# Optimization experiments

Hardware: AMD Instinct MI355X
Metric: run time of the kernel (lower is better)

Reference implementation:

```python
import jax, jax.numpy as jnp
import numpy as np

D = 64      # voxel grid resolution
N = 65536   # active voxels
C = 512     # channels
H = 2048    # mlp hidden = 4*C
EPS = 1e-6


def setup_inputs() -> dict:
    key = jax.random.key(0)
    ks = jax.random.split(key, 8)
    # unique sparse voxel coords (submanifold conv assumes no duplicates)
    rng = np.random.default_rng(0)
    lin = rng.choice(D * D * D, size=N, replace=False)
    coords = jnp.asarray(np.stack([lin // (D * D), (lin // D) % D, lin % D], axis=1), dtype=jnp.int32)  # [N,3]
    s = 1.0 / np.sqrt(C)
    return {
        'feats': jax.random.normal(ks[0], (N, C), jnp.float32),
        'coords': coords,
        'conv_w': jax.random.normal(ks[1], (3, 3, 3, C, C), jnp.float32) * (s / np.sqrt(27.0)),
        'conv_b': jax.random.normal(ks[2], (C,), jnp.float32) * 0.02,
        'ln_g': jnp.ones((C,), jnp.float32),
        'ln_b': jnp.zeros((C,), jnp.float32),
        'w1': jax.random.normal(ks[3], (C, H), jnp.float32) * s,
        'b1': jnp.zeros((H,), jnp.float32),
        'w2': jax.random.normal(ks[4], (H, C), jnp.float32) * (1.0 / np.sqrt(H)),
        'b2': jnp.zeros((C,), jnp.float32),
    }


def _sparse_conv3x3x3(feats, coords, conv_w, conv_b):
    # submanifold sparse conv: out[i] = b + sum_{offsets} feats[nbr(i,off)] @ W[off]
    n = feats.shape[0]
    # padded dense index grid: grid[x+1,y+1,z+1] = voxel row index, -1 = empty
    grid = jnp.full((D + 2, D + 2, D + 2), -1, dtype=jnp.int32)
    grid = grid.at[coords[:, 0] + 1, coords[:, 1] + 1, coords[:, 2] + 1].set(
        jnp.arange(n, dtype=jnp.int32))
    h = jnp.broadcast_to(conv_b, feats.shape).astype(feats.dtype)
    for dx in (0, 1, 2):
        for dy in (0, 1, 2):
            for dz in (0, 1, 2):
                nbr = grid[coords[:, 0] + dx, coords[:, 1] + dy, coords[:, 2] + dz]  # [N]
                valid = (nbr >= 0)
                g = feats[jnp.where(valid, nbr, 0)] * valid[:, None].astype(feats.dtype)  # [N,C]
                h = h + g @ conv_w[dx, dy, dz]
    return h


def reference(feats, coords, conv_w, conv_b, ln_g, ln_b, w1, b1, w2, b2):
    h = _sparse_conv3x3x3(feats, coords, conv_w, conv_b)          # [N,C]
    # LayerNorm32: normalize in fp32, eps=1e-6, affine
    h32 = h.astype(jnp.float32)
    mu = jnp.mean(h32, axis=-1, keepdims=True)
    var = jnp.mean(jnp.square(h32 - mu), axis=-1, keepdims=True)
    nf = ((h32 - mu) * jax.lax.rsqrt(var + EPS) * ln_g + ln_b).astype(feats.dtype)
    # SiLU MLP + residual
    out = jax.nn.silu(nf @ w1 + b1) @ w2 + b2 + feats
    return out
```

## Files before the change

### kernel.cpp

```cpp
#include <hip/hip_runtime.h>

typedef __attribute__((ext_vector_type(8))) short short8;
typedef __attribute__((ext_vector_type(4))) float f32x4;
typedef __attribute__((ext_vector_type(4))) float f4v;
typedef unsigned short u16;
typedef unsigned int u32;

#define NPTS 65536
#define CCH 512
#define GDIM 66
#define GDIM2 (66*66)
#define CAPO 18432
#define TPO1 144

__device__ __forceinline__ u16 f2bf(float f) {
    u32 u = __builtin_bit_cast(u32, f);
    u32 r = (u + 0x7fffu + ((u >> 16) & 1u)) >> 16;
    return (u16)r;
}
__device__ __forceinline__ float bf2f(u16 h) {
    u32 u = ((u32)h) << 16;
    return __builtin_bit_cast(float, u);
}
__device__ __forceinline__ void gld16(const void* g, void* l) {
    __builtin_amdgcn_global_load_lds((const __attribute__((address_space(1))) void*)g,
                                     (__attribute__((address_space(3))) void*)l, 16, 0, 0);
}


__global__ void scatter_vox(const int* __restrict__ coords, int* __restrict__ grid) {
    int i = blockIdx.x * 256 + threadIdx.x;
    if (i < NPTS) {
        int c0 = coords[3*i], c1 = coords[3*i+1], c2 = coords[3*i+2];
        grid[(c0+1)*GDIM2 + (c1+1)*GDIM + (c2+1)] = i;
    }
}

__global__ void cast_bf16(const float* __restrict__ in, u16* __restrict__ out, int n8) {
    int i = blockIdx.x * 256 + threadIdx.x;
    if (i >= n8) return;
    f4v a = *(const f4v*)(in + (size_t)i*8);
    f4v b = *(const f4v*)(in + (size_t)i*8 + 4);
    short8 o;
    #pragma unroll
    for (int j = 0; j < 4; ++j) { o[j] = (short)f2bf(a[j]); o[j+4] = (short)f2bf(b[j]); }
    *(short8*)(out + (size_t)i*8) = o;
}

__global__ void transpose_cast(const float* __restrict__ in, u16* __restrict__ out,
                               int R, int Cc) {
    __shared__ float tile[32][33];
    size_t moff = (size_t)blockIdx.z * R * Cc;
    in += moff; out += moff;
    int tx = threadIdx.x, ty = threadIdx.y;
    #pragma unroll
    for (int j = 0; j < 4; ++j) {
        int r = blockIdx.y*32 + ty + j*8;
        int c = blockIdx.x*32 + tx;
        tile[ty + j*8][tx] = in[(size_t)r*Cc + c];
    }
    __syncthreads();
    #pragma unroll
    for (int j = 0; j < 4; ++j) {
        int orow = blockIdx.x*32 + ty + j*8;
        int ocol = blockIdx.y*32 + tx;
        out[(size_t)orow*R + ocol] = f2bf(tile[tx][ty + j*8]);
    }
}


__device__ __forceinline__ int nbr_lookup(const int* coords, const int* grid, int i, int o) {
    int dx = o / 9, dy = (o / 3) % 3, dz = o % 3;
    int c0 = coords[3*i], c1 = coords[3*i+1], c2 = coords[3*i+2];
    return grid[(c0+dx)*GDIM2 + (c1+dy)*GDIM + (c2+dz)];
}

__global__ __launch_bounds__(256) void count_valid(const int* __restrict__ coords,
        const int* __restrict__ grid, int* __restrict__ blockCnt) {
    int o1 = blockIdx.y;
    int o = o1 + (o1 >= 13);
    int i = blockIdx.x*256 + threadIdx.x;
    int v = nbr_lookup(coords, grid, i, o);
    unsigned long long b = __ballot(v >= 0);
    __shared__ int wc[4];
    if ((threadIdx.x & 63) == 0) wc[threadIdx.x >> 6] = __popcll(b);
    __syncthreads();
    if (threadIdx.x == 0)
        blockCnt[o1*256 + blockIdx.x] = wc[0]+wc[1]+wc[2]+wc[3];
}

__global__ __launch_bounds__(256) void scan_kernel(const int* __restrict__ blockCnt,
        int* __restrict__ blockOff, int* __restrict__ cnt) {
    int t = threadIdx.x, lane = t & 63, w = t >> 6;
    __shared__ int wsum[4];
    for (int o1 = 0; o1 < 26; ++o1) {
        int v = blockCnt[o1*256 + t];
        int x = v;
        #pragma unroll
        for (int s = 1; s < 64; s <<= 1) {
            int y = __shfl_up(x, s);
            if (lane >= s) x += y;
        }
        if (lane == 63) wsum[w] = x;
        __syncthreads();
        int base = 0;
        for (int k = 0; k < w; ++k) base += wsum[k];
        blockOff[o1*256 + t] = base + x - v;
        if (t == 255) cnt[o1] = base + x;
        __syncthreads();
    }
}

__global__ __launch_bounds__(256) void fill_kernel(const int* __restrict__ coords,
        const int* __restrict__ grid, const int* __restrict__ blockOff,
        int* __restrict__ srcIdx, int* __restrict__ posMap) {
    int o1 = blockIdx.y;
    int o = o1 + (o1 >= 13);
    int i = blockIdx.x*256 + threadIdx.x;
    int v = nbr_lookup(coords, grid, i, o);
    bool valid = v >= 0;
    unsigned long long b = __ballot(valid);
    int lane = threadIdx.x & 63, w = threadIdx.x >> 6;
    __shared__ int wc[4];
    if (lane == 0) wc[w] = __popcll(b);
    __syncthreads();
    int base = blockOff[o1*256 + blockIdx.x];
    for (int k = 0; k < w; ++k) base += wc[k];
    int pre = __popcll(b & ((1ull << lane) - 1ull));
    int pos = base + pre;
    bool ok = valid && pos < CAPO;
    if (ok) srcIdx[o1*CAPO + pos] = v;
    posMap[(size_t)o1*NPTS + i] = ok ? pos : -1;
}


template<int MODE, int NX>
__global__ __launch_bounds__(256, 4) void gemm128(
    const u16* __restrict__ A, int lda,
    const u16* __restrict__ BT, int ldb,
    int nT,
    const float* __restrict__ bias,
    const float* __restrict__ resid,
    float* __restrict__ outf, u16* __restrict__ outb, int ldout, int first)
{
    __shared__ __align__(1024) char ldsA[16384];
    __shared__ __align__(1024) char ldsB[16384];
    const int L = blockIdx.x;
    const int cx = L & 7, tt0 = L >> 3;
    const int bx = tt0 % NX;
    const int by = cx + 8 * (tt0 / NX);
    const int row0 = by * 128, col0 = bx * 128;

    const int t = threadIdx.x;
    const int w = t >> 6, lane = t & 63;
    const int wm = w >> 1, wn = w & 1;
    const int ccsrc = (lane & 7) ^ (lane >> 3);
    const int laneRow = lane >> 3;

    f32x4 acc[4][4] = {};

    const u16* aptr[4];
    const u16* bptr[4];
    #pragma unroll
    for (int it = 0; it < 4; ++it) {
        int r = w*32 + it*8 + laneRow;
        aptr[it] = A + (size_t)(row0 + r)*lda + ccsrc*8;
        bptr[it] = BT + (size_t)(col0 + r)*ldb + ccsrc*8;
    }

    #pragma unroll 1
    for (int ks = 0; ks < nT; ++ks) {
        int k0 = ks * 64;
        #pragma unroll
        for (int it = 0; it < 4; ++it) {
            int c = w*256 + it*64 + lane;
            gld16(aptr[it] + k0, ldsA + c*16);
            gld16(bptr[it] + k0, ldsB + c*16);
        }
        __syncthreads();
        #pragma unroll
        for (int kk = 0; kk < 2; ++kk) {
            short8 a[4], b[4];
            #pragma unroll
            for (int f = 0; f < 4; ++f) {
                int rowA = wm*64 + f*16 + (lane & 15);
                int ch = (kk*4 + (lane >> 4)) ^ (lane & 7);
                a[f] = *(const short8*)(void*)(ldsA + rowA*128 + ch*16);
                int rowB = wn*64 + f*16 + (lane & 15);
                b[f] = *(const short8*)(void*)(ldsB + rowB*128 + ch*16);
            }
            #pragma unroll
            for (int i = 0; i < 4; ++i)
                #pragma unroll
                for (int j = 0; j < 4; ++j)
                    acc[i][j] = __builtin_amdgcn_mfma_f32_16x16x32_bf16(a[i], b[j], acc[i][j], 0, 0, 0);
        }
        __syncthreads();
    }

    #pragma unroll
    for (int i = 0; i < 4; ++i) {
        int r = row0 + wm*64 + i*16 + (lane >> 4)*4;
        #pragma unroll
        for (int j = 0; j < 4; ++j) {
            int c = col0 + wn*64 + j*16 + (lane & 15);
            float bv = bias[c];
            #pragma unroll
            for (int q = 0; q < 4; ++q) {
                float v = acc[i][j][q];
                if constexpr (MODE == 1) {
                    float val = v + bv;
                    float sg = 1.f / (1.f + __expf(-val));
                    outb[(size_t)(r+q)*ldout + c] = f2bf(val * sg);
                } else if constexpr (MODE == 2) {
                    size_t ix = (size_t)(r+q)*512 + c;
                    outf[ix] = first ? (v + bv + resid[ix]) : (v + outf[ix]);
                } else {
                    outb[(size_t)(r+q)*ldout + c] = f2bf(v + bv);
                }
            }
        }
    }
}

__global__ __launch_bounds__(256, 4) void comp_gemm(
    const u16* __restrict__ fb,
    const int* __restrict__ srcIdx,
    const int* __restrict__ cnt,
    const u16* __restrict__ wcT,
    u16* __restrict__ comp,
    int o1base)
{
    __shared__ __align__(1024) char ldsA[16384];
    __shared__ __align__(1024) char ldsB[16384];
    const int L = blockIdx.x;
    const int cx = L & 7, tt0 = L >> 3;
    const int bx = tt0 & 3;
    const int y  = cx + 8 * (tt0 >> 2);
    const int o1loc = y / TPO1, mt = y % TPO1;
    const int o1 = o1base + o1loc;
    const int n = cnt[o1];
    if (mt * 128 >= n) return;
    const int o = o1 + (o1 >= 13);
    const int t = threadIdx.x;
    const int w = t >> 6, lane = t & 63;
    const int wm = w >> 1, wn = w & 1;
    const int col0 = bx * 128;
    const int ccsrc = (lane & 7) ^ (lane >> 3);
    const int laneRow = lane >> 3;

    const int* sIdx = srcIdx + o1*CAPO + mt*128;
    const u16* wb = wcT + ((size_t)o << 18);

    const u16* aptr[4];
    const u16* bptr[4];
    #pragma unroll
    for (int it = 0; it < 4; ++it) {
        int rloc = w*32 + it*8 + laneRow;
        int src = (mt*128 + rloc < n) ? sIdx[rloc] : NPTS;
        aptr[it] = fb + (size_t)src*512 + ccsrc*8;
        bptr[it] = wb + (size_t)(col0 + rloc)*512 + ccsrc*8;
    }

    f32x4 acc[4][4] = {};

    #pragma unroll 1
    for (int ks = 0; ks < 8; ++ks) {
        int k0 = ks * 64;
        #pragma unroll
        for (int it = 0; it < 4; ++it) {
            int c = w*256 + it*64 + lane;
            gld16(aptr[it] + k0, ldsA + c*16);
            gld16(bptr[it] + k0, ldsB + c*16);
        }
        __syncthreads();
        #pragma unroll
        for (int kk = 0; kk < 2; ++kk) {
            short8 a[4], b[4];
            #pragma unroll
            for (int f = 0; f < 4; ++f) {
                int rowA = wm*64 + f*16 + (lane & 15);
                int ch = (kk*4 + (lane >> 4)) ^ (lane & 7);
                a[f] = *(const short8*)(void*)(ldsA + rowA*128 + ch*16);
                int rowB = wn*64 + f*16 + (lane & 15);
                b[f] = *(const short8*)(void*)(ldsB + rowB*128 + ch*16);
            }
            #pragma unroll
            for (int i = 0; i < 4; ++i)
                #pragma unroll
                for (int j = 0; j < 4; ++j)
                    acc[i][j] = __builtin_amdgcn_mfma_f32_16x16x32_bf16(a[i], b[j], acc[i][j], 0, 0, 0);
        }
        __syncthreads();
    }

    #pragma unroll
    for (int i = 0; i < 4; ++i) {
        #pragma unroll
        for (int q = 0; q < 4; ++q) {
            int rl = wm*64 + i*16 + (lane >> 4)*4 + q;
            if (mt*128 + rl < n) {
                u16* cr = comp + ((size_t)(o1loc*CAPO + mt*128 + rl))*512
                               + col0 + wn*64 + (lane & 15);
                #pragma unroll
                for (int j = 0; j < 4; ++j)
                    cr[j*16] = f2bf(acc[i][j][q]);
            }
        }
    }
}


template<int FINAL>
__global__ __launch_bounds__(512) void reduce_kernel(
    const u16* __restrict__ comp, const int* __restrict__ posMap,
    int o1base, int nOff,
    u16* __restrict__ h,
    const float* __restrict__ g, const float* __restrict__ bb,
    u16* __restrict__ nf)
{
    int w = threadIdx.x >> 6, lane = threadIdx.x & 63;
    int i = blockIdx.x*8 + w;
    u16* hr = h + (size_t)i*512 + lane*8;
    short8 hv = *(const short8*)hr;
    float x[8];
    #pragma unroll
    for (int j = 0; j < 8; ++j) x[j] = bf2f((u16)hv[j]);

    #pragma unroll 1
    for (int k = 0; k < nOff; ++k) {
        int pos = posMap[(size_t)(o1base + k)*NPTS + i];
        if (pos >= 0) {
            short8 cv = *(const short8*)(comp + ((size_t)(k*CAPO + pos))*512 + lane*8);
            #pragma unroll
            for (int j = 0; j < 8; ++j) x[j] += bf2f((u16)cv[j]);
        }
    }

    if constexpr (!FINAL) {
        short8 o;
        #pragma unroll
        for (int j = 0; j < 8; ++j) o[j] = (short)f2bf(x[j]);
        *(short8*)hr = o;
    } else {
        float s = 0.f, ss = 0.f;
        #pragma unroll
        for (int j = 0; j < 8; ++j) { s += x[j]; ss += x[j]*x[j]; }
        #pragma unroll
        for (int m = 1; m < 64; m <<= 1) { s += __shfl_xor(s, m); ss += __shfl_xor(ss, m); }
        float mu = s * (1.f/512.f);
        float var = ss * (1.f/512.f) - mu*mu;
        float inv = rsqrtf(var + 1e-6f);
        short8 o;
        #pragma unroll
        for (int j = 0; j < 8; ++j) {
            int c = lane*8 + j;
            o[j] = (short)f2bf((x[j] - mu) * inv * g[c] + bb[c]);
        }
        *(short8*)(nf + (size_t)i*512 + lane*8) = o;
    }
}


extern "C" void kernel_launch(void* const* d_in, const int* in_sizes, int n_in,
                              void* d_out, int out_size, void* d_ws, size_t ws_size,
                              hipStream_t stream) {
    const float* feats  = (const float*)d_in[0];
    const int*   coords = (const int*)d_in[1];
    const float* conv_w = (const float*)d_in[2];
    const float* conv_b = (const float*)d_in[3];
    const float* ln_g   = (const float*)d_in[4];
    const float* ln_b   = (const float*)d_in[5];
    const float* w1     = (const float*)d_in[6];
    const float* b1     = (const float*)d_in[7];
    const float* w2     = (const float*)d_in[8];
    const float* b2     = (const float*)d_in[9];
    float* out = (float*)d_out;
    char* ws = (char*)d_ws;

    size_t off = 0;
    auto take = [&](size_t bytes) -> void* {
        void* p = ws + off;
        off += (bytes + 1023) & ~(size_t)1023;
        return p;
    };
    int* grid_i   = (int*)take((size_t)GDIM*GDIM2*4);
    u16* wcT      = (u16*)take(27ull*512*512*2);
    u16* w1T      = (u16*)take(2048ull*512*2);
    u16* w2T      = (u16*)take(512ull*2048*2);
    u16* fb       = (u16*)take((NPTS+1ull)*512*2);
    int* srcIdx   = (int*)take(26ull*CAPO*4);
    int* posMap   = (int*)take(26ull*NPTS*4);
    int* blockCnt = (int*)take(26*256*4);
    int* blockOff = (int*)take(26*256*4);
    int* cnt      = (int*)take(26*4);
    u16* comp     = (u16*)take(13ull*CAPO*512*2);
    u16* h        = (u16*)take(67108864ull);
    u16* g1 = h;
    bool fused = (off + 201326592ull) <= ws_size;
    if (fused) take(201326592ull);
    else       take(67108864ull);
    u16* nf = fb;

    hipMemsetAsync(grid_i, 0xFF, (size_t)GDIM*GDIM2*4, stream);
    hipMemsetAsync(fb + (size_t)NPTS*512, 0, 512*2, stream);

    scatter_vox<<<NPTS/256, 256, 0, stream>>>(coords, grid_i);
    cast_bf16<<<(NPTS*CCH/8)/256, 256, 0, stream>>>(feats, fb, NPTS*CCH/8);
    transpose_cast<<<dim3(16,16,27), dim3(32,8), 0, stream>>>(conv_w, wcT, 512, 512);
    transpose_cast<<<dim3(64,16,1),  dim3(32,8), 0, stream>>>(w1, w1T, 512, 2048);
    transpose_cast<<<dim3(16,64,1),  dim3(32,8), 0, stream>>>(w2, w2T, 2048, 512);

    count_valid<<<dim3(256,26), 256, 0, stream>>>(coords, grid_i, blockCnt);
    scan_kernel<<<1, 256, 0, stream>>>(blockCnt, blockOff, cnt);
    fill_kernel<<<dim3(256,26), 256, 0, stream>>>(coords, grid_i, blockOff, srcIdx, posMap);

    gemm128<3,4><<<2048, 256, 0, stream>>>(
        fb, 512, wcT + (13ull << 18), 512, 8, conv_b, nullptr, nullptr, h, 512, 0);

    comp_gemm<<<4*TPO1*13, 256, 0, stream>>>(fb, srcIdx, cnt, wcT, comp, 0);
    reduce_kernel<0><<<NPTS/8, 512, 0, stream>>>(comp, posMap, 0, 13, h, nullptr, nullptr, nullptr);
    comp_gemm<<<4*TPO1*13, 256, 0, stream>>>(fb, srcIdx, cnt, wcT, comp, 13);
    reduce_kernel<1><<<NPTS/8, 512, 0, stream>>>(comp, posMap, 13, 13, h, ln_g, ln_b, nf);

    if (fused) {
        gemm128<1,16><<<8192, 256, 0, stream>>>(
            nf, 512, w1T, 512, 8, b1, nullptr, nullptr, g1, 2048, 0);
        gemm128<2,4><<<2048, 256, 0, stream>>>(
            g1, 2048, w2T, 2048, 32, b2, feats, out, nullptr, 512, 1);
    } else {
        for (int half = 0; half < 2; ++half) {
            gemm128<1,8><<<4096, 256, 0, stream>>>(
                nf, 512, w1T + (size_t)half*1024*512, 512, 8,
                b1 + half*1024, nullptr, nullptr, g1, 1024, 0);
            gemm128<2,4><<<2048, 256, 0, stream>>>(
                g1, 1024, w2T + half*1024, 2048, 16,
                b2, feats, out, nullptr, 512, half == 0);
        }
    }
}
```

Before: 1.118 ms.

## Reuse comp buffer for MLP hidden, read bf16 residual, parallelize scan

Reorganizes workspace so the MLP hidden activation aliases the conv partial buffer, letting the single fused W1/W2 path run without needing extra memory. When space allows, the normalized features get their own buffer and the final GEMM reads the residual from the bf16 feature copy rather than fp32 feats, cutting residual read bandwidth at some precision cost. The prefix scan is split across 26 blocks instead of one serial loop, and GEMM launch bounds are raised to target more resident blocks, which may force register spilling.

```diff
diff --git a/kernel.cpp b/kernel.cpp
--- a/kernel.cpp
+++ b/kernel.cpp
@@ -91,24 +91,22 @@
 
 __global__ __launch_bounds__(256) void scan_kernel(const int* __restrict__ blockCnt,
         int* __restrict__ blockOff, int* __restrict__ cnt) {
+    int o1 = blockIdx.x;
     int t = threadIdx.x, lane = t & 63, w = t >> 6;
     __shared__ int wsum[4];
-    for (int o1 = 0; o1 < 26; ++o1) {
-        int v = blockCnt[o1*256 + t];
-        int x = v;
-        #pragma unroll
-        for (int s = 1; s < 64; s <<= 1) {
-            int y = __shfl_up(x, s);
-            if (lane >= s) x += y;
-        }
-        if (lane == 63) wsum[w] = x;
-        __syncthreads();
-        int base = 0;
-        for (int k = 0; k < w; ++k) base += wsum[k];
-        blockOff[o1*256 + t] = base + x - v;
-        if (t == 255) cnt[o1] = base + x;
-        __syncthreads();
-    }
+    int v = blockCnt[o1*256 + t];
+    int x = v;
+    #pragma unroll
+    for (int s = 1; s < 64; s <<= 1) {
+        int y = __shfl_up(x, s);
+        if (lane >= s) x += y;
+    }
+    if (lane == 63) wsum[w] = x;
+    __syncthreads();
+    int base = 0;
+    for (int k = 0; k < w; ++k) base += wsum[k];
+    blockOff[o1*256 + t] = base + x - v;
+    if (t == 255) cnt[o1] = base + x;
 }
 
 __global__ __launch_bounds__(256) void fill_kernel(const int* __restrict__ coords,
@@ -134,14 +132,15 @@
 }
 
 
-template<int MODE, int NX>
-__global__ __launch_bounds__(256, 4) void gemm128(
+template<int MODE, int NX, int RES>
+__global__ __launch_bounds__(256, 5) void gemm128(
     const u16* __restrict__ A, int lda,
     const u16* __restrict__ BT, int ldb,
     int nT,
     const float* __restrict__ bias,
-    const float* __restrict__ resid,
-    float* __restrict__ outf, u16* __restrict__ outb, int ldout, int first)
+    const u16* __restrict__ fbres,
+    const float* __restrict__ fres,
+    float* __restrict__ outf, u16* __restrict__ outb, int ldout)
 {
     __shared__ __align__(1024) char ldsA[16384];
     __shared__ __align__(1024) char ldsB[16384];
@@ -214,7 +213,8 @@
                     outb[(size_t)(r+q)*ldout + c] = f2bf(val * sg);
                 } else if constexpr (MODE == 2) {
                     size_t ix = (size_t)(r+q)*512 + c;
-                    outf[ix] = first ? (v + bv + resid[ix]) : (v + outf[ix]);
+                    float rsd = RES ? bf2f(fbres[ix]) : fres[ix];
+                    outf[ix] = v + bv + rsd;
                 } else {
                     outb[(size_t)(r+q)*ldout + c] = f2bf(v + bv);
                 }
@@ -223,7 +223,7 @@
     }
 }
 
-__global__ __launch_bounds__(256, 4) void comp_gemm(
+__global__ __launch_bounds__(256, 5) void comp_gemm(
     const u16* __restrict__ fb,
     const int* __restrict__ srcIdx,
     const int* __restrict__ cnt,
@@ -315,13 +315,13 @@
 __global__ __launch_bounds__(512) void reduce_kernel(
     const u16* __restrict__ comp, const int* __restrict__ posMap,
     int o1base, int nOff,
-    u16* __restrict__ h,
+    u16* __restrict__ hc,
     const float* __restrict__ g, const float* __restrict__ bb,
     u16* __restrict__ nf)
 {
     int w = threadIdx.x >> 6, lane = threadIdx.x & 63;
     int i = blockIdx.x*8 + w;
-    u16* hr = h + (size_t)i*512 + lane*8;
+    u16* hr = hc + (size_t)i*512 + lane*8;
     short8 hv = *(const short8*)hr;
     float x[8];
     #pragma unroll
@@ -331,7 +331,7 @@
     for (int k = 0; k < nOff; ++k) {
         int pos = posMap[(size_t)(o1base + k)*NPTS + i];
         if (pos >= 0) {
-            short8 cv = *(const short8*)(comp + ((size_t)(k*CAPO + pos))*512 + lane*8);
+            short8 cv = *(const short8*)(comp + ((size_t)k*CAPO + pos)*512 + lane*8);
             #pragma unroll
             for (int j = 0; j < 8; ++j) x[j] += bf2f((u16)cv[j]);
         }
@@ -394,13 +394,18 @@
     int* blockCnt = (int*)take(26*256*4);
     int* blockOff = (int*)take(26*256*4);
     int* cnt      = (int*)take(26*4);
-    u16* comp     = (u16*)take(13ull*CAPO*512*2);
-    u16* h        = (u16*)take(67108864ull);
-    u16* g1 = h;
-    bool fused = (off + 201326592ull) <= ws_size;
-    if (fused) take(201326592ull);
-    else       take(67108864ull);
-    u16* nf = fb;
+
+    const size_t nf_b     = 67108864ull;
+    const size_t comp13_b = 13ull*CAPO*512*2;
+    const size_t hc_b     = 67108864ull;
+    const size_t slack    = 65536;
+
+    bool sepNF = (off + nf_b + comp13_b + hc_b + slack) <= ws_size;
+
+    u16* nf   = sepNF ? (u16*)take(nf_b) : fb;
+    u16* comp = (u16*)take(comp13_b);
+    u16* hc   = (u16*)take(hc_b);
+    u16* g1   = comp;
 
     hipMemsetAsync(grid_i, 0xFF, (size_t)GDIM*GDIM2*4, stream);
     hipMemsetAsync(fb + (size_t)NPTS*512, 0, 512*2, stream);
@@ -412,30 +417,26 @@
     transpose_cast<<<dim3(16,64,1),  dim3(32,8), 0, stream>>>(w2, w2T, 2048, 512);
 
     count_valid<<<dim3(256,26), 256, 0, stream>>>(coords, grid_i, blockCnt);
-    scan_kernel<<<1, 256, 0, stream>>>(blockCnt, blockOff, cnt);
+    scan_kernel<<<26, 256, 0, stream>>>(blockCnt, blockOff, cnt);
     fill_kernel<<<dim3(256,26), 256, 0, stream>>>(coords, grid_i, blockOff, srcIdx, posMap);
 
-    gemm128<3,4><<<2048, 256, 0, stream>>>(
-        fb, 512, wcT + (13ull << 18), 512, 8, conv_b, nullptr, nullptr, h, 512, 0);
+    gemm128<3,4,0><<<2048, 256, 0, stream>>>(
+        fb, 512, wcT + (13ull << 18), 512, 8, conv_b,
+        nullptr, nullptr, nullptr, hc, 512);
 
     comp_gemm<<<4*TPO1*13, 256, 0, stream>>>(fb, srcIdx, cnt, wcT, comp, 0);
-    reduce_kernel<0><<<NPTS/8, 512, 0, stream>>>(comp, posMap, 0, 13, h, nullptr, nullptr, nullptr);
+    reduce_kernel<0><<<NPTS/8, 512, 0, stream>>>(comp, posMap, 0, 13, hc, nullptr, nullptr, nullptr);
     comp_gemm<<<4*TPO1*13, 256, 0, stream>>>(fb, srcIdx, cnt, wcT, comp, 13);
-    reduce_kernel<1><<<NPTS/8, 512, 0, stream>>>(comp, posMap, 13, 13, h, ln_g, ln_b, nf);
-
-    if (fused) {
-        gemm128<1,16><<<8192, 256, 0, stream>>>(
-            nf, 512, w1T, 512, 8, b1, nullptr, nullptr, g1, 2048, 0);
-        gemm128<2,4><<<2048, 256, 0, stream>>>(
-            g1, 2048, w2T, 2048, 32, b2, feats, out, nullptr, 512, 1);
+    reduce_kernel<1><<<NPTS/8, 512, 0, stream>>>(comp, posMap, 13, 13, hc, ln_g, ln_b, nf);
+
+    gemm128<1,16,0><<<8192, 256, 0, stream>>>(
+        nf, 512, w1T, 512, 8, b1, nullptr, nullptr, nullptr, g1, 2048);
+
+    if (sepNF) {
+        gemm128<2,4,1><<<2048, 256, 0, stream>>>(
+            g1, 2048, w2T, 2048, 32, b2, fb, nullptr, out, nullptr, 512);
     } else {
-        for (int half = 0; half < 2; ++half) {
-            gemm128<1,8><<<4096, 256, 0, stream>>>(
-                nf, 512, w1T + (size_t)half*1024*512, 512, 8,
-                b1 + half*1024, nullptr, nullptr, g1, 1024, 0);
-            gemm128<2,4><<<2048, 256, 0, stream>>>(
-                g1, 1024, w2T + half*1024, 2048, 16,
-                b2, feats, out, nullptr, 512, half == 0);
-        }
-    }
-}
+        gemm128<2,4,0><<<2048, 256, 0, stream>>>(
+            g1, 2048, w2T, 2048, 32, b2, nullptr, feats, out, nullptr, 512);
+    }
+}
```

Result: slower. 1.445 ms (+29.3%).
